# Performance work log

Measured on AMD Instinct MI355X. Metric: run time of the kernel, lower is better.

## Reference

```python
import jax, jax.numpy as jnp
import numpy as np

N_LEVELS = 16
F_PER_LEVEL = 2
LOG2_T = 19
TABLE = 1 << LOG2_T
BASE_RES = 16.0
FINEST_RES = 512.0
PRIMES = jnp.array([1, 2654435761, 805459861, 3674653429, 2097192037, 1434869437], dtype=jnp.uint32)
# Hashing offsets: BOX_OFFSETS_6D enumerates dim0 in the OUTERMOST loop -> dim d uses bit (5-d) of vertex index.
OFF_HASH = jnp.array(((np.arange(64)[:, None] >> (5 - np.arange(6))) & 1).astype(np.int32))
# Interpolation weights use LSB-first bits (vertex_binary = [i >> d & 1]) -- faithful to the source (incl. its bit-order mismatch).
OFF_W = jnp.array(((np.arange(64)[:, None] >> np.arange(6)) & 1).astype(np.bool_))


def _hash6(coords):
    # coords: [..., 6] int32 -> int32 indices in [0, 2^19). uint32 wraparound matches torch int32 overflow + bitmask.
    u = coords.astype(jnp.uint32) * PRIMES
    h = u[..., 0]
    for d in range(1, 6):
        h = h ^ u[..., d]
    return (h & jnp.uint32(TABLE - 1)).astype(jnp.int32)


def _encode_level(emb, res, x):
    # emb: [T, F], res: scalar resolution, x: [B, 6] clamped to [0,1] box
    grid = 1.0 / res
    bl = jnp.floor(x * res).astype(jnp.int32)            # bottom-left voxel index, [B, 6]
    vmin = bl.astype(x.dtype) * grid                     # voxel_min_vertex
    w = jnp.clip((x - vmin) / (grid + 1e-6), 0.0, 1.0)   # [B, 6]
    verts = bl[:, None, :] + OFF_HASH[None]              # [B, 64, 6]
    ve = emb[_hash6(verts)]                              # gather: [B, 64, F]
    wv = jnp.where(OFF_W[None], w[:, None, :], 1.0 - w[:, None, :]).prod(-1)  # [B, 64]
    return jnp.einsum('bv,bvf->bf', wv, ve)


def hash_encode(x, embeddings):
    b = np.exp((np.log(FINEST_RES) - np.log(BASE_RES)) / (N_LEVELS - 1))
    res = jnp.maximum(jnp.floor(BASE_RES * b ** jnp.arange(N_LEVELS, dtype=jnp.float32)), 1.0)
    xc = jnp.clip(x, 0.0, 1.0)

    def body(carry, lv):
        emb, r = lv
        return carry, _encode_level(emb, r, xc)

    _, feats = jax.lax.scan(body, 0, (embeddings, res))  # [L, B, F]
    return jnp.transpose(feats, (1, 0, 2)).reshape(x.shape[0], N_LEVELS * F_PER_LEVEL)


def _mlp(W0, b0, Wres, bres, scales, Wout, bout, h):
    # NeRF_MLP_Residual_Scaled: initial -> (num_layers-1) scaled residual blocks -> output
    h = jax.nn.relu(h @ W0 + b0)
    for i in range(Wres.shape[0]):
        h = scales[i] * jax.nn.relu(h @ Wres[i] + bres[i]) + h
    return h @ Wout + bout


def setup_inputs() -> dict:
    key = jax.random.key(0)
    ks = jax.random.split(key, 10)
    B, C, H, IN, OUT = 524288, 4, 256, 32, 1
    NB = 3  # num_layers - 1 residual blocks
    x = jax.random.uniform(ks[0], (B, 6), jnp.float32)
    layer_id = jax.random.randint(ks[1], (B,), 0, C)
    embeddings = jax.random.uniform(ks[2], (N_LEVELS, TABLE, F_PER_LEVEL), jnp.float32, -1e-4, 1e-4)
    W0 = jax.random.normal(ks[3], (C, IN, H), jnp.float32) / np.sqrt(IN)
    b0 = jax.random.normal(ks[4], (C, H), jnp.float32) * 0.01
    Wres = jax.random.normal(ks[5], (C, NB, H, H), jnp.float32) / np.sqrt(H)
    bres = jax.random.normal(ks[6], (C, NB, H), jnp.float32) * 0.01
    scales = jax.random.normal(ks[7], (C, NB), jnp.float32) * 0.1
    Wout = jax.random.normal(ks[8], (C, H, OUT), jnp.float32) / np.sqrt(H)
    bout = jax.random.normal(ks[9], (C, OUT), jnp.float32) * 0.01
    return dict(x_6d_input=x, layer_id=layer_id, embeddings=embeddings, W0=W0, b0=b0,
                Wres=Wres, bres=bres, scales=scales, Wout=Wout, bout=bout)


def reference(x_6d_input, layer_id, embeddings, W0, b0, Wres, bres, scales, Wout, bout):
    enc = hash_encode(x_6d_input, embeddings)  # [B, 32]
    outs = jax.vmap(_mlp, in_axes=(0, 0, 0, 0, 0, 0, 0, None))(W0, b0, Wres, bres, scales, Wout, bout, enc)  # [C, B, out]
    midx = (layer_id % outs.shape[0]).astype(jnp.int32)
    return jnp.take_along_axis(outs, midx[None, :, None], axis=0)[0]  # [B, out]
```

## Files before the change

kernel.cpp:

```cpp
#include <hip/hip_runtime.h>
#include <stdint.h>

#define HTABLE (1u << 19)
#define TMASK  (HTABLE - 1u)
#define TILE   64
#define KSTR   264
#define KE     40

typedef __attribute__((ext_vector_type(8))) short short8;
typedef __attribute__((ext_vector_type(4))) float floatx4;

__device__ __forceinline__ float relu_(float v) { return fmaxf(v, 0.f); }

__device__ __forceinline__ uint32_t f2bf(float f) {
    uint32_t u = __float_as_uint(f);
    return (u + 0x7FFFu + ((u >> 16) & 1u)) >> 16;
}
__device__ __forceinline__ float bf2f(uint32_t h) { return __uint_as_float(h << 16); }

__device__ __forceinline__ uint32_t sel4(const uint4& v, uint32_t i) {
    uint32_t lo = (i & 1u) ? v.y : v.x;
    uint32_t hi = (i & 1u) ? v.w : v.z;
    return (i & 2u) ? hi : lo;
}

__device__ __constant__ uint32_t PRS[6] = {1u, 2654435761u, 805459861u, 3674653429u, 2097192037u, 1434869437u};
__device__ __constant__ float RESF[16]  = {16.f,20.f,25.f,32.f,40.f,50.f,64.f,80.f,101.f,128.f,161.f,203.f,256.f,322.f,406.f,512.f};
__device__ __constant__ float GRIDF[16] = {1.f/16.f,1.f/20.f,1.f/25.f,1.f/32.f,1.f/40.f,1.f/50.f,1.f/64.f,1.f/80.f,
                                           1.f/101.f,1.f/128.f,1.f/161.f,1.f/203.f,1.f/256.f,1.f/322.f,1.f/406.f,1.f/512.f};

__global__ void k_count(const int* __restrict__ lid, int n, int* __restrict__ cnt) {
    __shared__ int h4[4];
    int i = blockIdx.x * blockDim.x + threadIdx.x;
    if (threadIdx.x < 4) h4[threadIdx.x] = 0;
    __syncthreads();
    if (i < n) atomicAdd(&h4[lid[i] & 3], 1);
    __syncthreads();
    if (threadIdx.x < 4) atomicAdd(&cnt[threadIdx.x], h4[threadIdx.x]);
}

__global__ void k_offsets(const int* __restrict__ cnt, int* __restrict__ cursor) {
    if (threadIdx.x == 0 && blockIdx.x == 0) {
        int off = 0;
        for (int k = 0; k < 4; k++) {
            cursor[k] = off;
            off = (off + cnt[k] + 63) & ~63;
        }
    }
}

__global__ void k_scatter(const int* __restrict__ lid, int n, int* __restrict__ cursor, int* __restrict__ perm) {
    int i = blockIdx.x * blockDim.x + threadIdx.x;
    if (i >= n) return;
    int lane = threadIdx.x & 63;
    int c = lid[i] & 3;
    unsigned long long m0 = __ballot(c == 0), m1 = __ballot(c == 1);
    unsigned long long m2 = __ballot(c == 2), m3 = __ballot(c == 3);
    unsigned long long mc = (c == 0) ? m0 : (c == 1) ? m1 : (c == 2) ? m2 : m3;
    int rank = __popcll(mc & ((1ull << lane) - 1ull));
    int cntl = (lane == 0) ? __popcll(m0) : (lane == 1) ? __popcll(m1) : (lane == 2) ? __popcll(m2) : __popcll(m3);
    int basev = 0;
    if (lane < 4) basev = atomicAdd(&cursor[lane], cntl);
    int base = __shfl(basev, c, 64);
    perm[base + rank] = i;
}

__global__ __launch_bounds__(256) void k_packtab(const float* __restrict__ emb, uint32_t* __restrict__ T) {
    const int i = blockIdx.x * 256 + threadIdx.x;
    float2 e = ((const float2*)emb)[i];
    T[i] = f2bf(e.x) | (f2bf(e.y) << 16);
}

__global__ __launch_bounds__(256) void k_prep(const float* __restrict__ Wres, const float* __restrict__ W0,
                                              uint16_t* __restrict__ Wrt, uint16_t* __restrict__ W0t) {
    __shared__ float sm[64 * 65 > 32 * 257 ? 64 * 65 : 32 * 257];
    const int t = threadIdx.x;
    const int bid = blockIdx.x;
    if (bid < 192) {
        const int c = bid / 48, rem = bid % 48, ib = rem / 16, tile = rem % 16;
        const int n0 = (tile / 4) * 64, k0 = (tile % 4) * 64;
        const float* src = Wres + (size_t)(c * 3 + ib) * 65536;
        for (int i = 0; i < 16; i++) {
            int idx = t + 256 * i, r = idx >> 6, cc = idx & 63;
            sm[r * 65 + cc] = src[(size_t)(k0 + r) * 256 + n0 + cc];
        }
        __syncthreads();
        uint16_t* dst = Wrt + (size_t)(c * 3 + ib) * 65536;
        for (int i = 0; i < 16; i++) {
            int idx = t + 256 * i, rn = idx >> 6, ck = idx & 63;
            dst[(size_t)(n0 + rn) * 256 + k0 + ck] = (uint16_t)f2bf(sm[ck * 65 + rn]);
        }
    } else {
        const int c = bid - 192;
        for (int i = 0; i < 32; i++) {
            int idx = t + 256 * i, k = idx >> 8, n = idx & 255;
            sm[k * 257 + n] = W0[(size_t)c * 8192 + idx];
        }
        __syncthreads();
        for (int i = 0; i < 32; i++) {
            int idx = t + 256 * i, n = idx >> 5, k = idx & 31;
            W0t[(size_t)c * 8192 + idx] = (uint16_t)f2bf(sm[k * 257 + n]);
        }
    }
}

__global__ __launch_bounds__(256, 4) void k_encode(
    const float* __restrict__ x, const uint32_t* __restrict__ T,
    uint32_t* __restrict__ encP, int B)
{
    __shared__ float xs[256 * 6];
    const int t = threadIdx.x;
    const int NC8 = (B >> 8) << 3;
    const int pass = (blockIdx.x >= NC8) ? 1 : 0;
    const int rem  = blockIdx.x - pass * NC8;
    const int l    = (rem & 7) + (pass << 3);
    const int chunk = rem >> 3;
    const int pbase = chunk << 8;

    for (int idx = t; idx < 256 * 6; idx += 256) {
        float v = x[(size_t)pbase * 6 + idx];
        xs[idx] = fminf(fmaxf(v, 0.f), 1.f);
    }
    __syncthreads();

    const float res  = RESF[l];
    const float grid = GRIDF[l];
    float wv[6]; uint32_t ua[6], ub[6];
    #pragma unroll
    for (int d = 0; d < 6; d++) {
        float xv  = xs[t * 6 + d];
        float blf = floorf(xv * res);
        float w   = (xv - blf * grid) / (grid + 1e-6f);
        wv[d] = fminf(fmaxf(w, 0.f), 1.f);
        uint32_t uu = (uint32_t)(int)blf * PRS[d];
        ua[d] = uu; ub[d] = uu + PRS[d];
    }
    uint32_t HK[4]; float WK[4];
    #pragma unroll
    for (int q = 0; q < 4; q++) {
        const int b1 = (q >> 1) & 1, bb = q & 1;
        HK[q] = (b1 ? ub[4] : ua[4]) ^ (bb ? ub[5] : ua[5]);
        WK[q] = (bb ? wv[0] : 1.f - wv[0]) * (b1 ? wv[1] : 1.f - wv[1]);
    }
    uint32_t S8[8]; float W8[8];
    #pragma unroll
    for (int jj = 0; jj < 8; jj++) {
        const int j1 = jj >> 2, j = jj & 3;
        const int b1 = (j >> 1) & 1, bb = j & 1;
        const uint32_t hj = (b1 ? ub[2] : ua[2]) ^ (bb ? ub[3] : ua[3]);
        const float  wj = ((bb ? wv[2] : 1.f - wv[2]) * (b1 ? wv[3] : 1.f - wv[3]));
        S8[jj] = (j1 ? ub[1] : ua[1]) ^ hj;
        W8[jj] = (j1 ? wv[4] : 1.f - wv[4]) * wj;
    }
    const float w5a = 1.f - wv[5], w5b = wv[5];
    const uint32_t bl0  = ua[0];
    const uint32_t mask = bl0 ^ (bl0 + 1u);
    const uint32_t* __restrict__ Tl  = T + (size_t)l * HTABLE;
    const uint4*    __restrict__ Tl4 = reinterpret_cast<const uint4*>(Tl);

    float f0 = 0.f, f1 = 0.f;
    #pragma unroll 2
    for (int jj = 0; jj < 8; jj++) {
        const uint32_t Sj = S8[jj];
        const float   wj = W8[jj];
        #pragma unroll
        for (int k = 0; k < 4; k++) {
            const uint32_t h  = (bl0 ^ Sj ^ HK[k]) & TMASK;
            const float wS = wj * WK[k];
            uint32_t pa, pb;
            if (mask == 1u) {
                const uint2 pr = *(const uint2*)(Tl + (h & ~1u));
                pa = (h & 1u) ? pr.y : pr.x;
                pb = (h & 1u) ? pr.x : pr.y;
            } else if (mask == 3u) {
                const uint4 La = Tl4[h >> 2];
                const uint32_t i0 = h & 3u;
                pa = sel4(La, i0);
                pb = sel4(La, i0 ^ 3u);
            } else {
                pa = Tl[h];
                pb = Tl[h ^ mask];
            }
            const float e0x = __uint_as_float(pa << 16),  e0y = __uint_as_float(pa & 0xFFFF0000u);
            const float e1x = __uint_as_float(pb << 16),  e1y = __uint_as_float(pb & 0xFFFF0000u);
            f0 = fmaf(wS, fmaf(w5a, e0x, w5b * e1x), f0);
            f1 = fmaf(wS, fmaf(w5a, e0y, w5b * e1y), f1);
        }
    }
    encP[(size_t)l * B + pbase + t] = f2bf(f0) | (f2bf(f1) << 16);
}

__global__ __launch_bounds__(256, 2) void k_mlp2(
    const int* __restrict__ lid, const uint32_t* __restrict__ encP,
    const uint16_t* __restrict__ W0t, const float* __restrict__ b0,
    const uint16_t* __restrict__ Wrt, const float* __restrict__ bres,
    const float* __restrict__ scales, const float* __restrict__ Wout, const float* __restrict__ bout,
    const int* __restrict__ perm, float* __restrict__ out, int B)
{
    __shared__ uint16_t hB[64 * KSTR];
    __shared__ uint16_t encB[64 * KE];
    __shared__ float    bs[256];
    __shared__ float    outP[256];
    __shared__ int      permL[TILE];

    const int t  = threadIdx.x;
    const int lane = t & 63;
    const int wv = t >> 6;
    const int mi = lane & 15;
    const int q  = lane >> 4;

    if (t < TILE) permL[t] = perm[(size_t)blockIdx.x * TILE + t];
    __syncthreads();
    const int g0 = permL[0];
    if (g0 < 0) return;
    const int c = lid[g0] & 3;

    bs[t] = b0[c * 256 + t];
    for (int idx = t; idx < 16 * 64; idx += 256) {
        const int l = idx >> 6, pp = idx & 63;
        const int gi = permL[pp];
        ((uint32_t*)encB)[pp * (KE / 2) + l] = (gi >= 0) ? encP[(size_t)l * B + gi] : 0u;
    }
    __syncthreads();

    floatx4 acc[4][4];
    floatx4 h_reg[4][4];

    {
        #pragma unroll
        for (int mt = 0; mt < 4; mt++)
            #pragma unroll
            for (int nt = 0; nt < 4; nt++) acc[mt][nt] = (floatx4){0.f, 0.f, 0.f, 0.f};
        const short8* Wp = (const short8*)(W0t + (size_t)c * 8192);
        short8 A[4], Bf[4];
        #pragma unroll
        for (int mt = 0; mt < 4; mt++) A[mt] = Wp[(wv * 64 + mt * 16 + mi) * 4 + q];
        #pragma unroll
        for (int nt = 0; nt < 4; nt++) Bf[nt] = *(const short8*)&encB[(nt * 16 + mi) * KE + q * 8];
        #pragma unroll
        for (int mt = 0; mt < 4; mt++)
            #pragma unroll
            for (int nt = 0; nt < 4; nt++)
                acc[mt][nt] = __builtin_amdgcn_mfma_f32_16x16x32_bf16(A[mt], Bf[nt], acc[mt][nt], 0, 0, 0);
        #pragma unroll
        for (int mt = 0; mt < 4; mt++) {
            const int nb = wv * 64 + mt * 16 + q * 4;
            #pragma unroll
            for (int nt = 0; nt < 4; nt++) {
                floatx4 u = acc[mt][nt], h;
                h[0] = relu_(u[0] + bs[nb + 0]); h[1] = relu_(u[1] + bs[nb + 1]);
                h[2] = relu_(u[2] + bs[nb + 2]); h[3] = relu_(u[3] + bs[nb + 3]);
                h_reg[mt][nt] = h;
                uint2 pk; pk.x = f2bf(h[0]) | (f2bf(h[1]) << 16); pk.y = f2bf(h[2]) | (f2bf(h[3]) << 16);
                *(uint2*)&hB[(nt * 16 + mi) * KSTR + nb] = pk;
            }
        }
    }
    __syncthreads();

    #pragma unroll 1
    for (int ib = 0; ib < 3; ib++) {
        bs[t] = bres[(size_t)((c * 3 + ib) << 8) + t];
        const float s = scales[c * 3 + ib];
        #pragma unroll
        for (int mt = 0; mt < 4; mt++)
            #pragma unroll
            for (int nt = 0; nt < 4; nt++) acc[mt][nt] = (floatx4){0.f, 0.f, 0.f, 0.f};

        const short8* Wp = (const short8*)(Wrt + (size_t)(c * 3 + ib) * 65536);
        short8 Acur[4], Anext[4], Bf[4];
        #pragma unroll
        for (int mt = 0; mt < 4; mt++) Acur[mt] = Wp[(wv * 64 + mt * 16 + mi) * 32 + q];
        #pragma unroll 1
        for (int ks = 0; ks < 8; ks++) {
            #pragma unroll
            for (int nt = 0; nt < 4; nt++)
                Bf[nt] = *(const short8*)&hB[(nt * 16 + mi) * KSTR + ks * 32 + q * 8];
            if (ks < 7) {
                #pragma unroll
                for (int mt = 0; mt < 4; mt++)
                    Anext[mt] = Wp[(wv * 64 + mt * 16 + mi) * 32 + (ks + 1) * 4 + q];
            }
            #pragma unroll
            for (int mt = 0; mt < 4; mt++)
                #pragma unroll
                for (int nt = 0; nt < 4; nt++)
                    acc[mt][nt] = __builtin_amdgcn_mfma_f32_16x16x32_bf16(Acur[mt], Bf[nt], acc[mt][nt], 0, 0, 0);
            #pragma unroll
            for (int mt = 0; mt < 4; mt++) Acur[mt] = Anext[mt];
        }
        __syncthreads();
        #pragma unroll
        for (int mt = 0; mt < 4; mt++) {
            const int nb = wv * 64 + mt * 16 + q * 4;
            #pragma unroll
            for (int nt = 0; nt < 4; nt++) {
                floatx4 u = acc[mt][nt];
                floatx4 h = h_reg[mt][nt];
                h[0] = fmaf(s, relu_(u[0] + bs[nb + 0]), h[0]);
                h[1] = fmaf(s, relu_(u[1] + bs[nb + 1]), h[1]);
                h[2] = fmaf(s, relu_(u[2] + bs[nb + 2]), h[2]);
                h[3] = fmaf(s, relu_(u[3] + bs[nb + 3]), h[3]);
                h_reg[mt][nt] = h;
                if (ib < 2) {
                    uint2 pk; pk.x = f2bf(h[0]) | (f2bf(h[1]) << 16); pk.y = f2bf(h[2]) | (f2bf(h[3]) << 16);
                    *(uint2*)&hB[(nt * 16 + mi) * KSTR + nb] = pk;
                }
            }
        }
        if (ib < 2) __syncthreads();
    }

    __syncthreads();
    bs[t] = Wout[c * 256 + t];
    __syncthreads();
    float po[4] = {0.f, 0.f, 0.f, 0.f};
    #pragma unroll
    for (int mt = 0; mt < 4; mt++) {
        const int nb = wv * 64 + mt * 16 + q * 4;
        const float w0v = bs[nb + 0], w1v = bs[nb + 1], w2v = bs[nb + 2], w3v = bs[nb + 3];
        #pragma unroll
        for (int nt = 0; nt < 4; nt++) {
            const floatx4 h = h_reg[mt][nt];
            po[nt] += h[0] * w0v + h[1] * w1v + h[2] * w2v + h[3] * w3v;
        }
    }
    #pragma unroll
    for (int nt = 0; nt < 4; nt++) {
        float v = po[nt];
        v += __shfl_xor(v, 16, 64);
        v += __shfl_xor(v, 32, 64);
        if (q == 0) outP[wv * 64 + nt * 16 + mi] = v;
    }
    __syncthreads();
    if (t < TILE) {
        float r = outP[t] + outP[64 + t] + outP[128 + t] + outP[192 + t] + bout[c];
        const int gi = permL[t];
        if (gi >= 0) out[gi] = r;
    }
}

extern "C" void kernel_launch(void* const* d_in, const int* in_sizes, int n_in,
                              void* d_out, int out_size, void* d_ws, size_t ws_size,
                              hipStream_t stream) {
    const float* x      = (const float*)d_in[0];
    const int*   lid    = (const int*)  d_in[1];
    const float* emb    = (const float*)d_in[2];
    const float* W0     = (const float*)d_in[3];
    const float* b0     = (const float*)d_in[4];
    const float* Wres   = (const float*)d_in[5];
    const float* bres   = (const float*)d_in[6];
    const float* scales = (const float*)d_in[7];
    const float* Wout   = (const float*)d_in[8];
    const float* bout   = (const float*)d_in[9];
    float* out = (float*)d_out;

    const int B = in_sizes[1];
    int* cnt    = (int*)d_ws;
    int* cursor = cnt + 4;
    int* perm   = cnt + 64;
    uint16_t* W0t = (uint16_t*)((char*)d_ws + 2228224);
    uint16_t* Wrt = (uint16_t*)((char*)d_ws + 2359296);
    uint32_t* encP = (uint32_t*)((char*)d_ws + (4u << 20));
    uint32_t* T    = (uint32_t*)((char*)d_ws + (36u << 20));
    const int nblk = B / TILE + 4;

    (void)hipMemsetAsync(d_ws, 0, 32, stream);
    (void)hipMemsetAsync(perm, 0xFF, (size_t)nblk * TILE * sizeof(int), stream);
    k_packtab<<<(16 * (int)HTABLE) / 256, 256, 0, stream>>>(emb, T);
    k_prep   <<<196, 256, 0, stream>>>(Wres, W0, Wrt, W0t);
    k_count  <<<B / 256, 256, 0, stream>>>(lid, B, cnt);
    k_offsets<<<1, 64, 0, stream>>>(cnt, cursor);
    k_scatter<<<B / 256, 256, 0, stream>>>(lid, B, cursor, perm);
    k_encode <<<(B / 256) * 16, 256, 0, stream>>>(x, T, encP, B);
    k_mlp2   <<<nblk, 256, 0, stream>>>(lid, encP, W0t, b0, Wrt, bres, scales, Wout, bout, perm, out, B);
}
```

Measured before the change: 1.757 ms.

## Double MLP tile to 128 points with 512 threads, merge prep kernels

The MLP kernel now handles 128 points per block with 8 waves. Two point-groups of four waves share each block, so each wave's weight-fragment loads from global memory are amortized over twice as many points. The perm memset and the layer-id count kernel are folded into the table-packing kernel as extra block ranges, which removes a memset and a launch. The larger tile raises shared memory per block and may lower occupancy. Padding per class grows to 128, which adds some wasted rows.

```diff
diff --git a/kernel.cpp b/kernel.cpp
--- a/kernel.cpp
+++ b/kernel.cpp
@@ -3,7 +3,7 @@
 
 #define HTABLE (1u << 19)
 #define TMASK  (HTABLE - 1u)
-#define TILE   64
+#define TILE2  128
 #define KSTR   264
 #define KE     40
 
@@ -16,7 +16,6 @@
     uint32_t u = __float_as_uint(f);
     return (u + 0x7FFFu + ((u >> 16) & 1u)) >> 16;
 }
-__device__ __forceinline__ float bf2f(uint32_t h) { return __uint_as_float(h << 16); }
 
 __device__ __forceinline__ uint32_t sel4(const uint4& v, uint32_t i) {
     uint32_t lo = (i & 1u) ? v.y : v.x;
@@ -29,14 +28,27 @@
 __device__ __constant__ float GRIDF[16] = {1.f/16.f,1.f/20.f,1.f/25.f,1.f/32.f,1.f/40.f,1.f/50.f,1.f/64.f,1.f/80.f,
                                            1.f/101.f,1.f/128.f,1.f/161.f,1.f/203.f,1.f/256.f,1.f/322.f,1.f/406.f,1.f/512.f};
 
-__global__ void k_count(const int* __restrict__ lid, int n, int* __restrict__ cnt) {
-    __shared__ int h4[4];
-    int i = blockIdx.x * blockDim.x + threadIdx.x;
-    if (threadIdx.x < 4) h4[threadIdx.x] = 0;
-    __syncthreads();
-    if (i < n) atomicAdd(&h4[lid[i] & 3], 1);
-    __syncthreads();
-    if (threadIdx.x < 4) atomicAdd(&cnt[threadIdx.x], h4[threadIdx.x]);
+__global__ __launch_bounds__(256) void k_packtab(const float* __restrict__ emb, uint32_t* __restrict__ T,
+                                                 int* __restrict__ perm, int permN4,
+                                                 const int* __restrict__ lid, int n, int* __restrict__ cnt) {
+    const int bid = blockIdx.x;
+    const int t = threadIdx.x;
+    if (bid < 32768) {
+        const int i = bid * 256 + t;
+        float2 e = ((const float2*)emb)[i];
+        T[i] = f2bf(e.x) | (f2bf(e.y) << 16);
+    } else if (bid < 33281) {
+        const int i = (bid - 32768) * 256 + t;
+        if (i < permN4) ((int4*)perm)[i] = make_int4(-1, -1, -1, -1);
+    } else {
+        __shared__ int h4[4];
+        const int i = (bid - 33281) * 256 + t;
+        if (t < 4) h4[t] = 0;
+        __syncthreads();
+        if (i < n) atomicAdd(&h4[lid[i] & 3], 1);
+        __syncthreads();
+        if (t < 4) atomicAdd(&cnt[t], h4[t]);
+    }
 }
 
 __global__ void k_offsets(const int* __restrict__ cnt, int* __restrict__ cursor) {
@@ -44,7 +56,7 @@
         int off = 0;
         for (int k = 0; k < 4; k++) {
             cursor[k] = off;
-            off = (off + cnt[k] + 63) & ~63;
+            off = (off + cnt[k] + 127) & ~127;
         }
     }
 }
@@ -63,12 +75,6 @@
     if (lane < 4) basev = atomicAdd(&cursor[lane], cntl);
     int base = __shfl(basev, c, 64);
     perm[base + rank] = i;
-}
-
-__global__ __launch_bounds__(256) void k_packtab(const float* __restrict__ emb, uint32_t* __restrict__ T) {
-    const int i = blockIdx.x * 256 + threadIdx.x;
-    float2 e = ((const float2*)emb)[i];
-    T[i] = f2bf(e.x) | (f2bf(e.y) << 16);
 }
 
 __global__ __launch_bounds__(256) void k_prep(const float* __restrict__ Wres, const float* __restrict__ W0,
@@ -190,34 +196,37 @@
     encP[(size_t)l * B + pbase + t] = f2bf(f0) | (f2bf(f1) << 16);
 }
 
-__global__ __launch_bounds__(256, 2) void k_mlp2(
+__global__ __launch_bounds__(512, 2) void k_mlp3(
     const int* __restrict__ lid, const uint32_t* __restrict__ encP,
     const uint16_t* __restrict__ W0t, const float* __restrict__ b0,
     const uint16_t* __restrict__ Wrt, const float* __restrict__ bres,
     const float* __restrict__ scales, const float* __restrict__ Wout, const float* __restrict__ bout,
     const int* __restrict__ perm, float* __restrict__ out, int B)
 {
-    __shared__ uint16_t hB[64 * KSTR];
-    __shared__ uint16_t encB[64 * KE];
+    __shared__ uint16_t hB[TILE2 * KSTR];
+    __shared__ uint16_t encB[TILE2 * KE];
     __shared__ float    bs[256];
-    __shared__ float    outP[256];
-    __shared__ int      permL[TILE];
+    __shared__ int      permL[TILE2];
+    float* const outF = (float*)encB;
 
     const int t  = threadIdx.x;
     const int lane = t & 63;
     const int wv = t >> 6;
+    const int pg = wv >> 2;
+    const int wn = wv & 3;
+    const int po = pg * 64;
     const int mi = lane & 15;
     const int q  = lane >> 4;
 
-    if (t < TILE) permL[t] = perm[(size_t)blockIdx.x * TILE + t];
+    if (t < TILE2) permL[t] = perm[(size_t)blockIdx.x * TILE2 + t];
     __syncthreads();
     const int g0 = permL[0];
     if (g0 < 0) return;
     const int c = lid[g0] & 3;
 
-    bs[t] = b0[c * 256 + t];
-    for (int idx = t; idx < 16 * 64; idx += 256) {
-        const int l = idx >> 6, pp = idx & 63;
+    if (t < 256) bs[t] = b0[c * 256 + t];
+    for (int idx = t; idx < 16 * TILE2; idx += 512) {
+        const int l = idx >> 7, pp = idx & 127;
         const int gi = permL[pp];
         ((uint32_t*)encB)[pp * (KE / 2) + l] = (gi >= 0) ? encP[(size_t)l * B + gi] : 0u;
     }
@@ -234,9 +243,9 @@
         const short8* Wp = (const short8*)(W0t + (size_t)c * 8192);
         short8 A[4], Bf[4];
         #pragma unroll
-        for (int mt = 0; mt < 4; mt++) A[mt] = Wp[(wv * 64 + mt * 16 + mi) * 4 + q];
-        #pragma unroll
-        for (int nt = 0; nt < 4; nt++) Bf[nt] = *(const short8*)&encB[(nt * 16 + mi) * KE + q * 8];
+        for (int mt = 0; mt < 4; mt++) A[mt] = Wp[(wn * 64 + mt * 16 + mi) * 4 + q];
+        #pragma unroll
+        for (int nt = 0; nt < 4; nt++) Bf[nt] = *(const short8*)&encB[(po + nt * 16 + mi) * KE + q * 8];
         #pragma unroll
         for (int mt = 0; mt < 4; mt++)
             #pragma unroll
@@ -244,7 +253,7 @@
                 acc[mt][nt] = __builtin_amdgcn_mfma_f32_16x16x32_bf16(A[mt], Bf[nt], acc[mt][nt], 0, 0, 0);
         #pragma unroll
         for (int mt = 0; mt < 4; mt++) {
-            const int nb = wv * 64 + mt * 16 + q * 4;
+            const int nb = wn * 64 + mt * 16 + q * 4;
             #pragma unroll
             for (int nt = 0; nt < 4; nt++) {
                 floatx4 u = acc[mt][nt], h;
@@ -252,7 +261,7 @@
                 h[2] = relu_(u[2] + bs[nb + 2]); h[3] = relu_(u[3] + bs[nb + 3]);
                 h_reg[mt][nt] = h;
                 uint2 pk; pk.x = f2bf(h[0]) | (f2bf(h[1]) << 16); pk.y = f2bf(h[2]) | (f2bf(h[3]) << 16);
-                *(uint2*)&hB[(nt * 16 + mi) * KSTR + nb] = pk;
+                *(uint2*)&hB[(po + nt * 16 + mi) * KSTR + nb] = pk;
             }
         }
     }
@@ -260,7 +269,7 @@
 
     #pragma unroll 1
     for (int ib = 0; ib < 3; ib++) {
-        bs[t] = bres[(size_t)((c * 3 + ib) << 8) + t];
+        if (t < 256) bs[t] = bres[(size_t)((c * 3 + ib) << 8) + t];
         const float s = scales[c * 3 + ib];
         #pragma unroll
         for (int mt = 0; mt < 4; mt++)
@@ -270,16 +279,16 @@
         const short8* Wp = (const short8*)(Wrt + (size_t)(c * 3 + ib) * 65536);
         short8 Acur[4], Anext[4], Bf[4];
         #pragma unroll
-        for (int mt = 0; mt < 4; mt++) Acur[mt] = Wp[(wv * 64 + mt * 16 + mi) * 32 + q];
+        for (int mt = 0; mt < 4; mt++) Acur[mt] = Wp[(wn * 64 + mt * 16 + mi) * 32 + q];
         #pragma unroll 1
         for (int ks = 0; ks < 8; ks++) {
             #pragma unroll
             for (int nt = 0; nt < 4; nt++)
-                Bf[nt] = *(const short8*)&hB[(nt * 16 + mi) * KSTR + ks * 32 + q * 8];
+                Bf[nt] = *(const short8*)&hB[(po + nt * 16 + mi) * KSTR + ks * 32 + q * 8];
             if (ks < 7) {
                 #pragma unroll
                 for (int mt = 0; mt < 4; mt++)
-                    Anext[mt] = Wp[(wv * 64 + mt * 16 + mi) * 32 + (ks + 1) * 4 + q];
+                    Anext[mt] = Wp[(wn * 64 + mt * 16 + mi) * 32 + (ks + 1) * 4 + q];
             }
             #pragma unroll
             for (int mt = 0; mt < 4; mt++)
@@ -292,7 +301,7 @@
         __syncthreads();
         #pragma unroll
         for (int mt = 0; mt < 4; mt++) {
-            const int nb = wv * 64 + mt * 16 + q * 4;
+            const int nb = wn * 64 + mt * 16 + q * 4;
             #pragma unroll
             for (int nt = 0; nt < 4; nt++) {
                 floatx4 u = acc[mt][nt];
@@ -304,7 +313,7 @@
                 h_reg[mt][nt] = h;
                 if (ib < 2) {
                     uint2 pk; pk.x = f2bf(h[0]) | (f2bf(h[1]) << 16); pk.y = f2bf(h[2]) | (f2bf(h[3]) << 16);
-                    *(uint2*)&hB[(nt * 16 + mi) * KSTR + nb] = pk;
+                    *(uint2*)&hB[(po + nt * 16 + mi) * KSTR + nb] = pk;
                 }
             }
         }
@@ -312,29 +321,32 @@
     }
 
     __syncthreads();
-    bs[t] = Wout[c * 256 + t];
-    __syncthreads();
-    float po[4] = {0.f, 0.f, 0.f, 0.f};
+    if (t < 256) bs[t] = Wout[c * 256 + t];
+    __syncthreads();
+    float po4[4] = {0.f, 0.f, 0.f, 0.f};
     #pragma unroll
     for (int mt = 0; mt < 4; mt++) {
-        const int nb = wv * 64 + mt * 16 + q * 4;
+        const int nb = wn * 64 + mt * 16 + q * 4;
         const float w0v = bs[nb + 0], w1v = bs[nb + 1], w2v = bs[nb + 2], w3v = bs[nb + 3];
         #pragma unroll
         for (int nt = 0; nt < 4; nt++) {
             const floatx4 h = h_reg[mt][nt];
-            po[nt] += h[0] * w0v + h[1] * w1v + h[2] * w2v + h[3] * w3v;
-        }
-    }
+            po4[nt] += h[0] * w0v + h[1] * w1v + h[2] * w2v + h[3] * w3v;
+        }
+    }
+    __syncthreads();
     #pragma unroll
     for (int nt = 0; nt < 4; nt++) {
-        float v = po[nt];
+        float v = po4[nt];
         v += __shfl_xor(v, 16, 64);
         v += __shfl_xor(v, 32, 64);
-        if (q == 0) outP[wv * 64 + nt * 16 + mi] = v;
-    }
-    __syncthreads();
-    if (t < TILE) {
-        float r = outP[t] + outP[64 + t] + outP[128 + t] + outP[192 + t] + bout[c];
+        if (q == 0) outF[wv * 64 + nt * 16 + mi] = v;
+    }
+    __syncthreads();
+    if (t < TILE2) {
+        const int pgp = t >> 6, pp = t & 63;
+        float r = outF[(pgp * 4 + 0) * 64 + pp] + outF[(pgp * 4 + 1) * 64 + pp]
+                + outF[(pgp * 4 + 2) * 64 + pp] + outF[(pgp * 4 + 3) * 64 + pp] + bout[c];
         const int gi = permL[t];
         if (gi >= 0) out[gi] = r;
     }
@@ -363,15 +375,14 @@
     uint16_t* Wrt = (uint16_t*)((char*)d_ws + 2359296);
     uint32_t* encP = (uint32_t*)((char*)d_ws + (4u << 20));
     uint32_t* T    = (uint32_t*)((char*)d_ws + (36u << 20));
-    const int nblk = B / TILE + 4;
+    const int nblk2 = B / TILE2 + 4;
+    const int permN = nblk2 * TILE2;
 
     (void)hipMemsetAsync(d_ws, 0, 32, stream);
-    (void)hipMemsetAsync(perm, 0xFF, (size_t)nblk * TILE * sizeof(int), stream);
-    k_packtab<<<(16 * (int)HTABLE) / 256, 256, 0, stream>>>(emb, T);
-    k_prep   <<<196, 256, 0, stream>>>(Wres, W0, Wrt, W0t);
-    k_count  <<<B / 256, 256, 0, stream>>>(lid, B, cnt);
+    k_packtab<<<35329, 256, 0, stream>>>(emb, T, perm, permN / 4, lid, B, cnt);
     k_offsets<<<1, 64, 0, stream>>>(cnt, cursor);
     k_scatter<<<B / 256, 256, 0, stream>>>(lid, B, cursor, perm);
+    k_prep   <<<196, 256, 0, stream>>>(Wres, W0, Wrt, W0t);
     k_encode <<<(B / 256) * 16, 256, 0, stream>>>(x, T, encP, B);
-    k_mlp2   <<<nblk, 256, 0, stream>>>(lid, encP, W0t, b0, Wrt, bres, scales, Wout, bout, perm, out, B);
-}
+    k_mlp3   <<<nblk2, 512, 0, stream>>>(lid, encP, W0t, b0, Wrt, bres, scales, Wout, bout, perm, out, B);
+}
```

After: 1.832 ms. 4.3% more time.
